# Performance work log

Measured on AMD Instinct MI355X. Metric: run time of the kernel, lower is better.

Reference implementation:

```python
import jax, jax.numpy as jnp
import numpy as np
import math

N_EMBD = 1024
N_HEAD = 16
N_CTX = 2048
SCALE = True
NEG = 1e10


def setup_inputs() -> dict:
    key = jax.random.key(0)
    ks = jax.random.split(key, 4)
    B, S = 2, 2048
    x = jax.random.normal(ks[0], (B, S, N_EMBD), dtype=jnp.float32)
    c_attn_w = jax.random.normal(ks[1], (N_EMBD, 3 * N_EMBD), dtype=jnp.float32) * 0.02
    c_attn_b = jnp.zeros((3 * N_EMBD,), dtype=jnp.float32)
    c_proj_w = jax.random.normal(ks[2], (N_EMBD, N_EMBD), dtype=jnp.float32) * 0.02
    c_proj_b = jnp.zeros((N_EMBD,), dtype=jnp.float32)
    return {"x": x, "c_attn_w": c_attn_w, "c_attn_b": c_attn_b,
            "c_proj_w": c_proj_w, "c_proj_b": c_proj_b}


def reference(x, c_attn_w, c_attn_b, c_proj_w, c_proj_b):
    B, S, D = x.shape
    H = N_HEAD
    hd = D // H
    qkv = x @ c_attn_w + c_attn_b                      # [B,S,3D]
    q, k, v = jnp.split(qkv, 3, axis=-1)
    # split heads -> [B,H,S,hd]
    q = q.reshape(B, S, H, hd).transpose(0, 2, 1, 3)
    k = k.reshape(B, S, H, hd).transpose(0, 2, 1, 3)
    v = v.reshape(B, S, H, hd).transpose(0, 2, 1, 3)
    w = jnp.einsum('bhqd,bhkd->bhqk', q, k)           # [B,H,S,S]
    if SCALE:
        w = w / math.sqrt(hd)
    # multiplicative causal mask trick: w*b - 1e10*(1-b)
    b = jnp.tril(jnp.ones((S, S), dtype=w.dtype))[None, None]
    w = w * b - NEG * (1.0 - b)
    w = jax.nn.softmax(w, axis=-1)
    a = jnp.einsum('bhqk,bhkd->bhqd', w, v)           # [B,H,S,hd]
    a = a.transpose(0, 2, 1, 3).reshape(B, S, D)      # merge heads
    a = a @ c_proj_w + c_proj_b
    present = jnp.stack((k, v))                       # [2,B,H,S,hd]
    return a, present
```

## Files before the change

### kernel.cpp

```cpp
#include <hip/hip_runtime.h>
#include <hip/hip_bf16.h>
#include <cstdint>
#include <cstddef>

#define SEQ 2048
#define DMODEL 1024
#define NHEAD 16
#define HDIM 64
#define MTOT 4096
#define NQKV 3072
#define KDIM 1024

#define OUT_K_BASE  4194304u
#define OUT_V_BASE  8388608u

#define QSCALE 0.18033688011112043f

typedef __attribute__((ext_vector_type(4))) float f32x4;
typedef __attribute__((ext_vector_type(8))) __bf16 bf16x8;
typedef __attribute__((ext_vector_type(8))) short s16x8;
typedef __attribute__((ext_vector_type(4))) short s16x4;
typedef __attribute__((ext_vector_type(2))) int i32x2;

static __device__ __forceinline__ unsigned short f2bf(float f) {
  unsigned int u = __builtin_bit_cast(unsigned int, f);
  u += 0x7FFFu + ((u >> 16) & 1u);
  return (unsigned short)(u >> 16);
}

static __device__ __forceinline__ float bf2f(unsigned short u) {
  unsigned int x = ((unsigned int)u) << 16;
  return __builtin_bit_cast(float, x);
}

static __device__ __forceinline__ s16x4 pack4(float4 v) {
  s16x4 r;
  r[0] = (short)f2bf(v.x);
  r[1] = (short)f2bf(v.y);
  r[2] = (short)f2bf(v.z);
  r[3] = (short)f2bf(v.w);
  return r;
}

static __device__ __forceinline__ int cvtpk(float lo, float hi) {
  int r;
  asm("v_cvt_pk_bf16_f32 %0, %1, %2" : "=v"(r) : "v"(lo), "v"(hi));
  return r;
}

static __device__ __forceinline__ f32x4 mfma16(s16x8 a, s16x8 b, f32x4 c) {
  return __builtin_amdgcn_mfma_f32_16x16x32_bf16(
      __builtin_bit_cast(bf16x8, a), __builtin_bit_cast(bf16x8, b), c, 0, 0, 0);
}

static __device__ __forceinline__ void gload16(const void* g, void* l) {
  __builtin_amdgcn_global_load_lds(
      (const __attribute__((address_space(1))) unsigned int*)(uintptr_t)g,
      (__attribute__((address_space(3))) unsigned int*)(uintptr_t)l,
      16, 0, 0);
}

#define WAITVM(n) asm volatile("s_waitcnt vmcnt(" #n ")" ::: "memory")

__global__ __launch_bounds__(256) void convert_x(
    const float* __restrict__ X, unsigned short* __restrict__ Xbf)
{
  int i = blockIdx.x * 256 + threadIdx.x;
  float4 v = reinterpret_cast<const float4*>(X)[i];
  reinterpret_cast<s16x4*>(Xbf)[i] = pack4(v);
}

__global__ __launch_bounds__(256) void convert_wt(
    const float* __restrict__ W, unsigned short* __restrict__ Wt, int N)
{
  __shared__ unsigned short t[64][72];
  const int n0 = blockIdx.x * 64, k0 = blockIdx.y * 64;
  const int tid = threadIdx.x;
#pragma unroll
  for (int i = 0; i < 4; ++i) {
    int f = tid + (i << 8);
    int r = f >> 4, c4 = (f & 15) << 2;
    float4 v = *reinterpret_cast<const float4*>(&W[(size_t)(k0 + r) * N + n0 + c4]);
    *reinterpret_cast<s16x4*>(&t[r][c4]) = pack4(v);
  }
  __syncthreads();
#pragma unroll
  for (int i = 0; i < 2; ++i) {
    int g = tid + (i << 8);
    int n = g >> 3, k8 = (g & 7) << 3;
    s16x8 o;
#pragma unroll
    for (int jj = 0; jj < 8; ++jj) o[jj] = (short)t[k8 + jj][n];
    *reinterpret_cast<s16x8*>(&Wt[(size_t)(n0 + n) * KDIM + k0 + k8]) = o;
  }
}

__global__ __launch_bounds__(256) void qkv_gemm(
    const unsigned short* __restrict__ Xbf,
    const unsigned short* __restrict__ Wt,
    const float* __restrict__ Bias,
    unsigned short* __restrict__ Qbf,
    unsigned short* __restrict__ Kbf,
    unsigned short* __restrict__ Vt,
    float* __restrict__ outp)
{
  __shared__ __align__(16) unsigned short lds_a[2][128][64];
  __shared__ __align__(16) unsigned short lds_b[2][128][64];

  const int tid = threadIdx.x;
  const int lane = tid & 63;
  const int wv = tid >> 6;
  const int wr = wv >> 1, wc = wv & 1;
  const int m0 = blockIdx.x * 128;
  const int n0 = blockIdx.y * 128;
  const int lr = lane & 15;
  const int gq = lane >> 4;

  const f32x4 fzero = {0.f, 0.f, 0.f, 0.f};
  f32x4 acc[4][4];
#pragma unroll
  for (int i = 0; i < 4; ++i)
#pragma unroll
    for (int j = 0; j < 4; ++j) acc[i][j] = fzero;

  {
    const int r0 = tid >> 3;
    const int c0 = tid & 7;
    auto stage = [&](int nb, int kk) {
#pragma unroll
      for (int i = 0; i < 4; ++i) {
        int r = r0 + (i << 5);
        int sc = ((c0 ^ (r & 7)) << 3);
        int ub = (((i << 8) + (wv << 6)) << 3);
        gload16(&Xbf[(size_t)(m0 + r) * KDIM + kk + sc], &lds_a[nb][0][0] + ub);
        gload16(&Wt[(size_t)(n0 + r) * KDIM + kk + sc], &lds_b[nb][0][0] + ub);
      }
    };
    stage(0, 0);
    stage(1, 64);
    for (int t = 0; t < 16; ++t) {
      if (t < 15) { WAITVM(8); } else { WAITVM(0); }
      __builtin_amdgcn_s_barrier();
      const int bufg = t & 1;
      __builtin_amdgcn_s_setprio(1);
#pragma unroll
      for (int kf = 0; kf < 2; ++kf) {
        s16x8 bfv[4];
#pragma unroll
        for (int ni = 0; ni < 4; ++ni) {
          int row = wc * 64 + ni * 16 + lr;
          bfv[ni] = *reinterpret_cast<const s16x8*>(
              &lds_b[bufg][row][((kf * 4 + gq) ^ (row & 7)) << 3]);
        }
#pragma unroll
        for (int mi = 0; mi < 4; ++mi) {
          int row = wr * 64 + mi * 16 + lr;
          s16x8 af = *reinterpret_cast<const s16x8*>(
              &lds_a[bufg][row][((kf * 4 + gq) ^ (row & 7)) << 3]);
#pragma unroll
          for (int ni = 0; ni < 4; ++ni)
            acc[mi][ni] = mfma16(af, bfv[ni], acc[mi][ni]);
        }
      }
      __builtin_amdgcn_s_setprio(0);
      __builtin_amdgcn_s_barrier();
      if (t < 14) stage(bufg, (t + 2) << 6);
    }
  }

  __syncthreads();
  unsigned short* T = (wv < 2) ? (&lds_a[0][0][0] + (wv << 12))
                               : (&lds_b[0][0][0] + ((wv - 2) << 12));
  const int seg = n0 >> 10;
  const int b = m0 >> 11;
  const int s0 = (m0 & 2047) + wr * 64;
  const int h = ((n0 & 1023) >> 6) + wc;
  const size_t bh = (size_t)(b * NHEAD + h);

  if (seg <= 1) {
#pragma unroll
    for (int ni = 0; ni < 4; ++ni) {
      int c = n0 + wc * 64 + ni * 16 + lr;
      float bias = Bias[c];
      int ch = 2 * ni + (lr >> 3);
      int el = lr & 7;
#pragma unroll
      for (int mi = 0; mi < 4; ++mi)
#pragma unroll
        for (int j = 0; j < 4; ++j) {
          int s_loc = mi * 16 + gq * 4 + j;
          float val = acc[mi][ni][j] + bias;
          if (seg == 0) val *= QSCALE;
          T[s_loc * 64 + ((ch ^ (s_loc & 7)) << 3) + el] = f2bf(val);
        }
    }
    unsigned short* dst = (seg == 0) ? Qbf : Kbf;
#pragma unroll
    for (int it = 0; it < 8; ++it) {
      int rr = (lane >> 3) + (it << 3);
      int cl = lane & 7;
      s16x8 vv = *reinterpret_cast<const s16x8*>(
          &T[rr * 64 + ((cl ^ (rr & 7)) << 3)]);
      size_t off = (bh * SEQ + s0 + rr) * HDIM + (cl << 3);
      *reinterpret_cast<s16x8*>(&dst[off]) = vv;
      if (seg == 1) {
        float4 lo = {bf2f((unsigned short)vv[0]), bf2f((unsigned short)vv[1]),
                     bf2f((unsigned short)vv[2]), bf2f((unsigned short)vv[3])};
        float4 hi = {bf2f((unsigned short)vv[4]), bf2f((unsigned short)vv[5]),
                     bf2f((unsigned short)vv[6]), bf2f((unsigned short)vv[7])};
        *reinterpret_cast<float4*>(&outp[OUT_K_BASE + off]) = lo;
        *reinterpret_cast<float4*>(&outp[OUT_K_BASE + off + 4]) = hi;
      }
    }
  } else {
#pragma unroll
    for (int ni = 0; ni < 4; ++ni) {
      int c = n0 + wc * 64 + ni * 16 + lr;
      float bias = Bias[c];
      int d_loc = ni * 16 + lr;
      int dsw = d_loc & 7;
#pragma unroll
      for (int mi = 0; mi < 4; ++mi)
#pragma unroll
        for (int j = 0; j < 4; ++j) {
          int s_loc = mi * 16 + gq * 4 + j;
          T[d_loc * 64 + (((s_loc >> 3) ^ dsw) << 3) + (s_loc & 7)] =
              f2bf(acc[mi][ni][j] + bias);
        }
    }
#pragma unroll
    for (int it = 0; it < 8; ++it) {
      int dl = (lane >> 3) + (it << 3);
      int cl = lane & 7;
      s16x8 vv = *reinterpret_cast<const s16x8*>(
          &T[dl * 64 + ((cl ^ (dl & 7)) << 3)]);
      *reinterpret_cast<s16x8*>(
          &Vt[(bh * HDIM + dl) * SEQ + s0 + (cl << 3)]) = vv;
    }
#pragma unroll
    for (int ni = 0; ni < 4; ++ni) {
      int c = n0 + wc * 64 + ni * 16 + lr;
      float bias = Bias[c];
      int ch = 2 * ni + (lr >> 3);
      int el = lr & 7;
#pragma unroll
      for (int mi = 0; mi < 4; ++mi)
#pragma unroll
        for (int j = 0; j < 4; ++j) {
          int s_loc = mi * 16 + gq * 4 + j;
          T[s_loc * 64 + ((ch ^ (s_loc & 7)) << 3) + el] =
              f2bf(acc[mi][ni][j] + bias);
        }
    }
#pragma unroll
    for (int it = 0; it < 8; ++it) {
      int rr = (lane >> 3) + (it << 3);
      int cl = lane & 7;
      s16x8 vv = *reinterpret_cast<const s16x8*>(
          &T[rr * 64 + ((cl ^ (rr & 7)) << 3)]);
      float4 lo = {bf2f((unsigned short)vv[0]), bf2f((unsigned short)vv[1]),
                   bf2f((unsigned short)vv[2]), bf2f((unsigned short)vv[3])};
      float4 hi = {bf2f((unsigned short)vv[4]), bf2f((unsigned short)vv[5]),
                   bf2f((unsigned short)vv[6]), bf2f((unsigned short)vv[7])};
      size_t off = (bh * SEQ + s0 + rr) * HDIM + (cl << 3);
      *reinterpret_cast<float4*>(&outp[OUT_V_BASE + off]) = lo;
      *reinterpret_cast<float4*>(&outp[OUT_V_BASE + off + 4]) = hi;
    }
  }
}

__global__ __launch_bounds__(256) void proj_gemm(
    const unsigned short* __restrict__ Abf,
    const unsigned short* __restrict__ Wpt,
    const float* __restrict__ Bias,
    float* __restrict__ out)
{
  __shared__ __align__(16) unsigned short lds_a[2][128][64];
  __shared__ __align__(16) unsigned short lds_b[2][128][64];

  const int tid = threadIdx.x;
  const int lane = tid & 63;
  const int wv = tid >> 6;
  const int wr = wv >> 1, wc = wv & 1;
  const int m0 = blockIdx.x * 128;
  const int n0 = blockIdx.y * 128;
  const int lr = lane & 15;
  const int gq = lane >> 4;

  const f32x4 fzero = {0.f, 0.f, 0.f, 0.f};
  f32x4 acc[4][4];
#pragma unroll
  for (int i = 0; i < 4; ++i)
#pragma unroll
    for (int j = 0; j < 4; ++j) acc[i][j] = fzero;

  {
    const int r0 = tid >> 3;
    const int c0 = tid & 7;
    auto stage = [&](int nb, int kk) {
#pragma unroll
      for (int i = 0; i < 4; ++i) {
        int r = r0 + (i << 5);
        int sc = ((c0 ^ (r & 7)) << 3);
        int ub = (((i << 8) + (wv << 6)) << 3);
        gload16(&Abf[(size_t)(m0 + r) * KDIM + kk + sc], &lds_a[nb][0][0] + ub);
        gload16(&Wpt[(size_t)(n0 + r) * KDIM + kk + sc], &lds_b[nb][0][0] + ub);
      }
    };
    stage(0, 0);
    stage(1, 64);
    for (int t = 0; t < 16; ++t) {
      if (t < 15) { WAITVM(8); } else { WAITVM(0); }
      __builtin_amdgcn_s_barrier();
      const int bufg = t & 1;
      __builtin_amdgcn_s_setprio(1);
#pragma unroll
      for (int kf = 0; kf < 2; ++kf) {
        s16x8 bfv[4];
#pragma unroll
        for (int ni = 0; ni < 4; ++ni) {
          int row = wc * 64 + ni * 16 + lr;
          bfv[ni] = *reinterpret_cast<const s16x8*>(
              &lds_b[bufg][row][((kf * 4 + gq) ^ (row & 7)) << 3]);
        }
#pragma unroll
        for (int mi = 0; mi < 4; ++mi) {
          int row = wr * 64 + mi * 16 + lr;
          s16x8 af = *reinterpret_cast<const s16x8*>(
              &lds_a[bufg][row][((kf * 4 + gq) ^ (row & 7)) << 3]);
#pragma unroll
          for (int ni = 0; ni < 4; ++ni)
            acc[mi][ni] = mfma16(af, bfv[ni], acc[mi][ni]);
        }
      }
      __builtin_amdgcn_s_setprio(0);
      __builtin_amdgcn_s_barrier();
      if (t < 14) stage(bufg, (t + 2) << 6);
    }
  }

#pragma unroll
  for (int ni = 0; ni < 4; ++ni) {
    int c = n0 + wc * 64 + ni * 16 + lr;
    float bias = Bias[c];
#pragma unroll
    for (int mi = 0; mi < 4; ++mi) {
#pragma unroll
      for (int j = 0; j < 4; ++j) {
        int m = m0 + wr * 64 + mi * 16 + gq * 4 + j;
        out[(size_t)m * DMODEL + c] = acc[mi][ni][j] + bias;
      }
    }
  }
}

__global__ __launch_bounds__(256) void attn_fwd(
    const unsigned short* __restrict__ Qbf,
    const unsigned short* __restrict__ Kbf,
    const unsigned short* __restrict__ Vtg,
    unsigned short* __restrict__ Abf)
{
  __shared__ __align__(16) unsigned short K_lds[2][64][64];
  __shared__ __align__(16) unsigned short V_lds[2][64][64];
  __shared__ __align__(16) unsigned short P_lds[4][16][64];

  const int tid = threadIdx.x;
  const int lane = tid & 63;
  const int wv = tid >> 6;
  const int bid = blockIdx.x;
  const int qt = 15 - (bid >> 5);
  const int bh = bid & 31;

  const int lr = lane & 15;
  const int gq = lane >> 4;

  const unsigned short* Kg = Kbf + (size_t)bh * (SEQ * HDIM);
  const unsigned short* Vg = Vtg + (size_t)bh * (SEQ * HDIM);
  const unsigned short* Qg = Qbf + (size_t)bh * (SEQ * HDIM)
                                 + (size_t)(qt * 128 + wv * 32) * HDIM;

  s16x8 qf0[2], qf1[2];
#pragma unroll
  for (int g = 0; g < 2; ++g) {
    qf0[g] = *reinterpret_cast<const s16x8*>(&Qg[(g * 16 + lr) * 64 + (gq << 3)]);
    qf1[g] = *reinterpret_cast<const s16x8*>(&Qg[(g * 16 + lr) * 64 + 32 + (gq << 3)]);
  }

  const f32x4 fzero = {0.f, 0.f, 0.f, 0.f};
  f32x4 O[2][4];
  float mrow[2] = {-1e30f, -1e30f}, lrow[2] = {0.f, 0.f};
#pragma unroll
  for (int g = 0; g < 2; ++g)
#pragma unroll
    for (int no = 0; no < 4; ++no) O[g][no] = fzero;

#define STAGE(kv0, nb)                                                        \
  {                                                                           \
    _Pragma("unroll")                                                         \
    for (int i = 0; i < 2; ++i) {                                             \
      int L = tid + (i << 8);                                                 \
      int r = L >> 3, c = L & 7;                                              \
      int cc = (c ^ (r & 7)) << 3;                                            \
      int ubase = ((i << 8) + (wv << 6)) << 3;                                \
      gload16(&Kg[(((kv0) + r) << 6) + cc], &K_lds[nb][0][0] + ubase);        \
      gload16(&Vg[((size_t)r << 11) + (kv0) + cc], &V_lds[nb][0][0] + ubase); \
    }                                                                         \
  }

  const int ntiles = qt * 2 + 2;
  STAGE(0, 0);

  for (int t = 0; t < ntiles; ++t) {
    __syncthreads();
    if (t < ntiles - 1) STAGE((t + 1) * 64, (t + 1) & 1);
    const int buf = t & 1;
    const bool needmask = (t >= 2 * qt);

#pragma unroll
    for (int g = 0; g < 2; ++g) {
      f32x4 sc[4];
#pragma unroll
      for (int ni = 0; ni < 4; ++ni) {
        int kr = ni * 16 + lr;
        int sw = kr & 7;
        s16x8 kb0 = *reinterpret_cast<const s16x8*>(&K_lds[buf][kr][(gq ^ sw) << 3]);
        s16x8 kb1 = *reinterpret_cast<const s16x8*>(&K_lds[buf][kr][((gq + 4) ^ sw) << 3]);
        f32x4 tacc = mfma16(kb0, qf0[g], fzero);
        sc[ni] = mfma16(kb1, qf1[g], tacc);
      }

      if (needmask) {
        int qgl = qt * 128 + wv * 32 + g * 16 + lr;
        int kvb = t * 64;
#pragma unroll
        for (int ni = 0; ni < 4; ++ni)
#pragma unroll
          for (int r = 0; r < 4; ++r)
            if (kvb + ni * 16 + gq * 4 + r > qgl) sc[ni][r] = -1e30f;
      }

      float tmax = fmaxf(fmaxf(fmaxf(sc[0][0], sc[0][1]), fmaxf(sc[0][2], sc[0][3])),
                         fmaxf(fmaxf(sc[1][0], sc[1][1]), fmaxf(sc[1][2], sc[1][3])));
      tmax = fmaxf(tmax,
                   fmaxf(fmaxf(fmaxf(sc[2][0], sc[2][1]), fmaxf(sc[2][2], sc[2][3])),
                         fmaxf(fmaxf(sc[3][0], sc[3][1]), fmaxf(sc[3][2], sc[3][3]))));
      tmax = fmaxf(tmax, __shfl_xor(tmax, 16));
      tmax = fmaxf(tmax, __shfl_xor(tmax, 32));
      float newm = fmaxf(mrow[g], tmax);
      float fs = __builtin_amdgcn_exp2f(mrow[g] - newm);
      mrow[g] = newm;
      float rs = 0.f;
#pragma unroll
      for (int ni = 0; ni < 4; ++ni) {
#pragma unroll
        for (int r = 0; r < 4; ++r) {
          float p = __builtin_amdgcn_exp2f(sc[ni][r] - newm);
          sc[ni][r] = p;
          rs += p;
        }
      }
      rs += __shfl_xor(rs, 16);
      rs += __shfl_xor(rs, 32);
      lrow[g] = lrow[g] * fs + rs;
#pragma unroll
      for (int no = 0; no < 4; ++no) O[g][no] *= fs;

      {
        unsigned short* Prow = &P_lds[wv][lr][0];
        const int swl = lr & 7;
#pragma unroll
        for (int ni = 0; ni < 4; ++ni) {
          i32x2 d2;
          d2[0] = cvtpk(sc[ni][0], sc[ni][1]);
          d2[1] = cvtpk(sc[ni][2], sc[ni][3]);
          int off = ((((2 * ni) + (gq >> 1)) ^ swl) << 3) + ((gq & 1) << 2);
          *reinterpret_cast<i32x2*>(&Prow[off]) = d2;
        }
        s16x8 pB0 = *reinterpret_cast<const s16x8*>(&Prow[(gq ^ swl) << 3]);
        s16x8 pB1 = *reinterpret_cast<const s16x8*>(&Prow[((gq + 4) ^ swl) << 3]);

#pragma unroll
        for (int no = 0; no < 4; ++no) {
          int dr = no * 16 + lr;
          int sw = dr & 7;
          s16x8 vb0 = *reinterpret_cast<const s16x8*>(&V_lds[buf][dr][(gq ^ sw) << 3]);
          s16x8 vb1 = *reinterpret_cast<const s16x8*>(&V_lds[buf][dr][((gq + 4) ^ sw) << 3]);
          O[g][no] = mfma16(vb0, pB0, O[g][no]);
          O[g][no] = mfma16(vb1, pB1, O[g][no]);
        }
      }
    }
  }

  const int b = bh >> 4, h = bh & 15;
#pragma unroll
  for (int g = 0; g < 2; ++g) {
    float inv = 1.0f / lrow[g];
    int srow = qt * 128 + wv * 32 + g * 16 + lr;
    size_t base = (size_t)(b * SEQ + srow) * DMODEL + h * 64 + (gq << 2);
#pragma unroll
    for (int no = 0; no < 4; ++no) {
      s16x4 ov;
#pragma unroll
      for (int r = 0; r < 4; ++r) ov[r] = (short)f2bf(O[g][no][r] * inv);
      *reinterpret_cast<s16x4*>(&Abf[base + no * 16]) = ov;
    }
  }
#undef STAGE
}

extern "C" void kernel_launch(void* const* d_in, const int* in_sizes, int n_in,
                              void* d_out, int out_size, void* d_ws, size_t ws_size,
                              hipStream_t stream) {
  const float* x        = (const float*)d_in[0];
  const float* c_attn_w = (const float*)d_in[1];
  const float* c_attn_b = (const float*)d_in[2];
  const float* c_proj_w = (const float*)d_in[3];
  const float* c_proj_b = (const float*)d_in[4];
  float* out = (float*)d_out;

  unsigned short* Qbf = (unsigned short*)d_ws;
  unsigned short* Xbf = Qbf + 4194304;
  unsigned short* Abf = Xbf;
  unsigned short* Wt  = Qbf + 8388608;
  unsigned short* Wpt = Wt;
  unsigned short* Kbf = (unsigned short*)out;
  unsigned short* Vt  = Kbf + 4194304;

  convert_x<<<dim3(4096), 256, 0, stream>>>(x, Xbf);
  convert_wt<<<dim3(48, 16), 256, 0, stream>>>(c_attn_w, Wt, NQKV);
  qkv_gemm<<<dim3(32, 24), 256, 0, stream>>>(Xbf, Wt, c_attn_b, Qbf, Kbf, Vt, out);
  convert_wt<<<dim3(16, 16), 256, 0, stream>>>(c_proj_w, Wpt, DMODEL);
  attn_fwd<<<dim3(512), 256, 0, stream>>>(Qbf, Kbf, Vt, Abf);
  proj_gemm<<<dim3(32, 8), 256, 0, stream>>>(Abf, Wpt, c_proj_b, out);
}
```

Measured before the change: 129.9 us.

## Halve attention query tile to 64 rows and double grid size

Each attention block now handles 64 query rows (16 per wave) instead of 128, so the grid doubles to 1024 blocks and only the diagonal tile needs causal masking. The point is more parallelism and finer causal load balance across the 256 CUs, plus fewer registers per wave, with launch bounds asking for 4 waves per SIMD. The cost is that each K/V tile staged into LDS is reused by half as many query rows, so global and LDS traffic per FLOP roughly doubles.

```diff
diff --git a/kernel.cpp b/kernel.cpp
--- a/kernel.cpp
+++ b/kernel.cpp
@@ -354,7 +354,7 @@
   }
 }
 
-__global__ __launch_bounds__(256) void attn_fwd(
+__global__ __launch_bounds__(256, 4) void attn_fwd(
     const unsigned short* __restrict__ Qbf,
     const unsigned short* __restrict__ Kbf,
     const unsigned short* __restrict__ Vtg,
@@ -368,7 +368,7 @@
   const int lane = tid & 63;
   const int wv = tid >> 6;
   const int bid = blockIdx.x;
-  const int qt = 15 - (bid >> 5);
+  const int qt = 31 - (bid >> 5);
   const int bh = bid & 31;
 
   const int lr = lane & 15;
@@ -377,22 +377,16 @@
   const unsigned short* Kg = Kbf + (size_t)bh * (SEQ * HDIM);
   const unsigned short* Vg = Vtg + (size_t)bh * (SEQ * HDIM);
   const unsigned short* Qg = Qbf + (size_t)bh * (SEQ * HDIM)
-                                 + (size_t)(qt * 128 + wv * 32) * HDIM;
-
-  s16x8 qf0[2], qf1[2];
-#pragma unroll
-  for (int g = 0; g < 2; ++g) {
-    qf0[g] = *reinterpret_cast<const s16x8*>(&Qg[(g * 16 + lr) * 64 + (gq << 3)]);
-    qf1[g] = *reinterpret_cast<const s16x8*>(&Qg[(g * 16 + lr) * 64 + 32 + (gq << 3)]);
-  }
+                                 + (size_t)(qt * 64 + wv * 16) * HDIM;
+
+  s16x8 qf0 = *reinterpret_cast<const s16x8*>(&Qg[lr * 64 + (gq << 3)]);
+  s16x8 qf1 = *reinterpret_cast<const s16x8*>(&Qg[lr * 64 + 32 + (gq << 3)]);
 
   const f32x4 fzero = {0.f, 0.f, 0.f, 0.f};
-  f32x4 O[2][4];
-  float mrow[2] = {-1e30f, -1e30f}, lrow[2] = {0.f, 0.f};
-#pragma unroll
-  for (int g = 0; g < 2; ++g)
-#pragma unroll
-    for (int no = 0; no < 4; ++no) O[g][no] = fzero;
+  f32x4 O[4];
+  float mrow = -1e30f, lrow = 0.f;
+#pragma unroll
+  for (int no = 0; no < 4; ++no) O[no] = fzero;
 
 #define STAGE(kv0, nb)                                                        \
   {                                                                           \
@@ -407,104 +401,95 @@
     }                                                                         \
   }
 
-  const int ntiles = qt * 2 + 2;
   STAGE(0, 0);
 
-  for (int t = 0; t < ntiles; ++t) {
+  for (int t = 0; t <= qt; ++t) {
     __syncthreads();
-    if (t < ntiles - 1) STAGE((t + 1) * 64, (t + 1) & 1);
+    if (t < qt) STAGE((t + 1) * 64, (t + 1) & 1);
     const int buf = t & 1;
-    const bool needmask = (t >= 2 * qt);
-
-#pragma unroll
-    for (int g = 0; g < 2; ++g) {
-      f32x4 sc[4];
+
+    f32x4 sc[4];
+#pragma unroll
+    for (int ni = 0; ni < 4; ++ni) {
+      int kr = ni * 16 + lr;
+      int sw = kr & 7;
+      s16x8 kb0 = *reinterpret_cast<const s16x8*>(&K_lds[buf][kr][(gq ^ sw) << 3]);
+      s16x8 kb1 = *reinterpret_cast<const s16x8*>(&K_lds[buf][kr][((gq + 4) ^ sw) << 3]);
+      f32x4 tacc = mfma16(kb0, qf0, fzero);
+      sc[ni] = mfma16(kb1, qf1, tacc);
+    }
+
+    if (t == qt) {
+      int qloc = wv * 16 + lr;
+#pragma unroll
+      for (int ni = 0; ni < 4; ++ni)
+#pragma unroll
+        for (int r = 0; r < 4; ++r)
+          if (ni * 16 + gq * 4 + r > qloc) sc[ni][r] = -1e30f;
+    }
+
+    float tmax = fmaxf(fmaxf(fmaxf(sc[0][0], sc[0][1]), fmaxf(sc[0][2], sc[0][3])),
+                       fmaxf(fmaxf(sc[1][0], sc[1][1]), fmaxf(sc[1][2], sc[1][3])));
+    tmax = fmaxf(tmax,
+                 fmaxf(fmaxf(fmaxf(sc[2][0], sc[2][1]), fmaxf(sc[2][2], sc[2][3])),
+                       fmaxf(fmaxf(sc[3][0], sc[3][1]), fmaxf(sc[3][2], sc[3][3]))));
+    tmax = fmaxf(tmax, __shfl_xor(tmax, 16));
+    tmax = fmaxf(tmax, __shfl_xor(tmax, 32));
+    float newm = fmaxf(mrow, tmax);
+    float fs = __builtin_amdgcn_exp2f(mrow - newm);
+    mrow = newm;
+    float rs = 0.f;
+#pragma unroll
+    for (int ni = 0; ni < 4; ++ni) {
+#pragma unroll
+      for (int r = 0; r < 4; ++r) {
+        float p = __builtin_amdgcn_exp2f(sc[ni][r] - newm);
+        sc[ni][r] = p;
+        rs += p;
+      }
+    }
+    rs += __shfl_xor(rs, 16);
+    rs += __shfl_xor(rs, 32);
+    lrow = lrow * fs + rs;
+#pragma unroll
+    for (int no = 0; no < 4; ++no) O[no] *= fs;
+
+    {
+      unsigned short* Prow = &P_lds[wv][lr][0];
+      const int swl = lr & 7;
 #pragma unroll
       for (int ni = 0; ni < 4; ++ni) {
-        int kr = ni * 16 + lr;
-        int sw = kr & 7;
-        s16x8 kb0 = *reinterpret_cast<const s16x8*>(&K_lds[buf][kr][(gq ^ sw) << 3]);
-        s16x8 kb1 = *reinterpret_cast<const s16x8*>(&K_lds[buf][kr][((gq + 4) ^ sw) << 3]);
-        f32x4 tacc = mfma16(kb0, qf0[g], fzero);
-        sc[ni] = mfma16(kb1, qf1[g], tacc);
-      }
-
-      if (needmask) {
-        int qgl = qt * 128 + wv * 32 + g * 16 + lr;
-        int kvb = t * 64;
-#pragma unroll
-        for (int ni = 0; ni < 4; ++ni)
-#pragma unroll
-          for (int r = 0; r < 4; ++r)
-            if (kvb + ni * 16 + gq * 4 + r > qgl) sc[ni][r] = -1e30f;
-      }
-
-      float tmax = fmaxf(fmaxf(fmaxf(sc[0][0], sc[0][1]), fmaxf(sc[0][2], sc[0][3])),
-                         fmaxf(fmaxf(sc[1][0], sc[1][1]), fmaxf(sc[1][2], sc[1][3])));
-      tmax = fmaxf(tmax,
-                   fmaxf(fmaxf(fmaxf(sc[2][0], sc[2][1]), fmaxf(sc[2][2], sc[2][3])),
-                         fmaxf(fmaxf(sc[3][0], sc[3][1]), fmaxf(sc[3][2], sc[3][3]))));
-      tmax = fmaxf(tmax, __shfl_xor(tmax, 16));
-      tmax = fmaxf(tmax, __shfl_xor(tmax, 32));
-      float newm = fmaxf(mrow[g], tmax);
-      float fs = __builtin_amdgcn_exp2f(mrow[g] - newm);
-      mrow[g] = newm;
-      float rs = 0.f;
-#pragma unroll
-      for (int ni = 0; ni < 4; ++ni) {
-#pragma unroll
-        for (int r = 0; r < 4; ++r) {
-          float p = __builtin_amdgcn_exp2f(sc[ni][r] - newm);
-          sc[ni][r] = p;
-          rs += p;
-        }
-      }
-      rs += __shfl_xor(rs, 16);
-      rs += __shfl_xor(rs, 32);
-      lrow[g] = lrow[g] * fs + rs;
-#pragma unroll
-      for (int no = 0; no < 4; ++no) O[g][no] *= fs;
-
-      {
-        unsigned short* Prow = &P_lds[wv][lr][0];
-        const int swl = lr & 7;
-#pragma unroll
-        for (int ni = 0; ni < 4; ++ni) {
-          i32x2 d2;
-          d2[0] = cvtpk(sc[ni][0], sc[ni][1]);
-          d2[1] = cvtpk(sc[ni][2], sc[ni][3]);
-          int off = ((((2 * ni) + (gq >> 1)) ^ swl) << 3) + ((gq & 1) << 2);
-          *reinterpret_cast<i32x2*>(&Prow[off]) = d2;
-        }
-        s16x8 pB0 = *reinterpret_cast<const s16x8*>(&Prow[(gq ^ swl) << 3]);
-        s16x8 pB1 = *reinterpret_cast<const s16x8*>(&Prow[((gq + 4) ^ swl) << 3]);
-
-#pragma unroll
-        for (int no = 0; no < 4; ++no) {
-          int dr = no * 16 + lr;
-          int sw = dr & 7;
-          s16x8 vb0 = *reinterpret_cast<const s16x8*>(&V_lds[buf][dr][(gq ^ sw) << 3]);
-          s16x8 vb1 = *reinterpret_cast<const s16x8*>(&V_lds[buf][dr][((gq + 4) ^ sw) << 3]);
-          O[g][no] = mfma16(vb0, pB0, O[g][no]);
-          O[g][no] = mfma16(vb1, pB1, O[g][no]);
-        }
+        i32x2 d2;
+        d2[0] = cvtpk(sc[ni][0], sc[ni][1]);
+        d2[1] = cvtpk(sc[ni][2], sc[ni][3]);
+        int off = ((((2 * ni) + (gq >> 1)) ^ swl) << 3) + ((gq & 1) << 2);
+        *reinterpret_cast<i32x2*>(&Prow[off]) = d2;
+      }
+      s16x8 pB0 = *reinterpret_cast<const s16x8*>(&Prow[(gq ^ swl) << 3]);
+      s16x8 pB1 = *reinterpret_cast<const s16x8*>(&Prow[((gq + 4) ^ swl) << 3]);
+
+#pragma unroll
+      for (int no = 0; no < 4; ++no) {
+        int dr = no * 16 + lr;
+        int sw = dr & 7;
+        s16x8 vb0 = *reinterpret_cast<const s16x8*>(&V_lds[buf][dr][(gq ^ sw) << 3]);
+        s16x8 vb1 = *reinterpret_cast<const s16x8*>(&V_lds[buf][dr][((gq + 4) ^ sw) << 3]);
+        O[no] = mfma16(vb0, pB0, O[no]);
+        O[no] = mfma16(vb1, pB1, O[no]);
       }
     }
   }
 
   const int b = bh >> 4, h = bh & 15;
-#pragma unroll
-  for (int g = 0; g < 2; ++g) {
-    float inv = 1.0f / lrow[g];
-    int srow = qt * 128 + wv * 32 + g * 16 + lr;
-    size_t base = (size_t)(b * SEQ + srow) * DMODEL + h * 64 + (gq << 2);
-#pragma unroll
-    for (int no = 0; no < 4; ++no) {
-      s16x4 ov;
-#pragma unroll
-      for (int r = 0; r < 4; ++r) ov[r] = (short)f2bf(O[g][no][r] * inv);
-      *reinterpret_cast<s16x4*>(&Abf[base + no * 16]) = ov;
-    }
+  float inv = 1.0f / lrow;
+  int srow = qt * 64 + wv * 16 + lr;
+  size_t base = (size_t)(b * SEQ + srow) * DMODEL + h * 64 + (gq << 2);
+#pragma unroll
+  for (int no = 0; no < 4; ++no) {
+    s16x4 ov;
+#pragma unroll
+    for (int r = 0; r < 4; ++r) ov[r] = (short)f2bf(O[no][r] * inv);
+    *reinterpret_cast<s16x4*>(&Abf[base + no * 16]) = ov;
   }
 #undef STAGE
 }
@@ -531,6 +516,6 @@
   convert_wt<<<dim3(48, 16), 256, 0, stream>>>(c_attn_w, Wt, NQKV);
   qkv_gemm<<<dim3(32, 24), 256, 0, stream>>>(Xbf, Wt, c_attn_b, Qbf, Kbf, Vt, out);
   convert_wt<<<dim3(16, 16), 256, 0, stream>>>(c_proj_w, Wpt, DMODEL);
-  attn_fwd<<<dim3(512), 256, 0, stream>>>(Qbf, Kbf, Vt, Abf);
+  attn_fwd<<<dim3(1024), 256, 0, stream>>>(Qbf, Kbf, Vt, Abf);
   proj_gemm<<<dim3(32, 8), 256, 0, stream>>>(Abf, Wpt, c_proj_b, out);
 }
```

Result: faster. 113.5 us (-12.6%).
